# Kernel tuning notes

Hardware: AMD Instinct MI355X
Metric: run time of the kernel (lower is better)

Reference implementation:

```python
import jax, jax.numpy as jnp
import numpy as np

D_MODEL = 512
TEMP = 30.0  # softmax temperature used by TransformerTrack-style RelationUnit
EPS = 1e-5
NORM_SCALE = float(np.sqrt(1.0 / (D_MODEL * 4 * 4)))


def _instance_l2norm(x):
    # x: [n, hw, b, d]; InstanceL2Norm over (dim, h, w) per (image, batch) sample
    n, hw, b, d = x.shape
    ss = jnp.sum(x * x, axis=(1, 3), keepdims=True)  # [n,1,b,1]
    return x * (NORM_SCALE * jnp.sqrt((d * hw) / (ss + EPS)))


def _cnorm(r, i):
    # joint L2 normalization of a complex vector along last axis
    s = jnp.sqrt(jnp.sum(r * r + i * i, axis=-1, keepdims=True) + 1e-12)
    return r / s, i / s


def _rel_self_attn(xr, xi, er, ei, WK):
    # xr/xi: [n, L, b, d]; er/ei: [n, L, L, b, dk] relative (helix) embeddings
    qr, qi = _cnorm(xr @ WK, xi @ WK)           # [n,L,b,dk]
    # real part of complex conjugate inner product <q, k>
    scores = (jnp.einsum('nqbk,nlbk->nbql', qr, qr)
              + jnp.einsum('nqbk,nlbk->nbql', qi, qi)
              + jnp.einsum('nqbk,nqlbk->nbql', qr, er)
              + jnp.einsum('nqbk,nqlbk->nbql', qi, ei))
    A = jax.nn.softmax(scores * TEMP, axis=-1)  # [n,b,q,l]
    out_r = jnp.einsum('nbql,nlbd->nqbd', A, xr)
    out_i = jnp.einsum('nbql,nlbd->nqbd', A, xi)
    return out_r, out_i


def _cross_attn(qr_in, qi_in, kr_in, ki_in, vr, vi, WK):
    # q: [Lq,b,d]; k,v: [Lk,b,d]
    qr, qi = _cnorm(qr_in @ WK, qi_in @ WK)
    kr, ki = _cnorm(kr_in @ WK, ki_in @ WK)
    scores = jnp.einsum('qbk,lbk->bql', qr, kr) + jnp.einsum('qbk,lbk->bql', qi, ki)
    A = jax.nn.softmax(scores * TEMP, axis=-1)
    out_r = jnp.einsum('bql,lbd->qbd', A, vr)
    out_i = jnp.einsum('bql,lbd->qbd', A, vi)
    return out_r, out_i


def _forward(src_real, src_imag, tgt_real, tgt_imag,
             src_emb_real, src_emb_imag, tgt_emb_real, tgt_emb_imag,
             pos_real, pos_imag, WK_rel, WK_cross):
    n, b, d, h, w = src_real.shape
    hw = h * w

    def tok(x):  # [n,b,d,h,w] -> [n,hw,b,d]
        return x.reshape(n, b, d, hw).transpose(0, 3, 1, 2)

    def emb(x):  # [n,b,dk,hw,hw] -> [n,hw,hw,b,dk]
        return x.transpose(0, 3, 4, 1, 2)

    sr, si = tok(src_real), tok(src_imag)
    tr, ti = tok(tgt_real), tok(tgt_imag)
    esr, esi = emb(src_emb_real), emb(src_emb_imag)
    etr, eti = emb(tgt_emb_real), emb(tgt_emb_imag)

    # ---- encoder (num_layers = 1) ----
    s2r, s2i = _rel_self_attn(sr, si, esr, esi, WK_rel)
    mem_r = _instance_l2norm(sr + s2r).reshape(n * hw, b, d)
    mem_i = _instance_l2norm(si + s2i).reshape(n * hw, b, d)

    # pos: [n,b,h,w] -> [n*hw, b, d] (broadcast over dim as in .repeat(1,1,dim))
    pr = jnp.broadcast_to(pos_real.reshape(n, b, hw).transpose(0, 2, 1).reshape(n * hw, b, 1), (n * hw, b, d))
    pi = jnp.broadcast_to(pos_imag.reshape(n, b, hw).transpose(0, 2, 1).reshape(n * hw, b, 1), (n * hw, b, d))

    def IN3(x):
        return _instance_l2norm(x.reshape(n, hw, b, d)).reshape(n * hw, b, d)

    # ---- decoder (num_layers = 1) ----
    t2r, t2i = _rel_self_attn(tr, ti, etr, eti, WK_rel)
    xr = _instance_l2norm(tr + t2r).reshape(n * hw, b, d)
    xi = _instance_l2norm(ti + t2i).reshape(n * hw, b, d)

    mask_r, mask_i = _cross_attn(xr, xi, mem_r, mem_i, pr, pi, WK_cross)
    y2r = IN3(xr * mask_r)
    y2i = IN3(xi * mask_i)

    t3r, t3i = _cross_attn(xr, xi, mem_r, mem_i, mem_r * pr, mem_i * pi, WK_cross)
    y4r = IN3(xr + t3r)
    y4i = IN3(xi + t3i)

    out_r = IN3(y2r + y4r)
    out_i = IN3(y2i + y4i)

    feat_r = out_r.reshape(n, h, w, b, d).transpose(0, 3, 4, 1, 2).reshape(n * b, d, h, w)
    feat_i = out_i.reshape(n, h, w, b, d).transpose(0, 3, 4, 1, 2).reshape(n * b, d, h, w)
    return out_r, out_i, feat_r, feat_i


def setup_inputs() -> dict:
    key = jax.random.key(0)
    ks = jax.random.split(key, 12)
    n, b, d, h, dk = 2, 2, 512, 16, 64
    hw = h * h
    inp = {
        'src_real': jax.random.normal(ks[0], (n, b, d, h, h), jnp.float32),
        'src_imag': jax.random.normal(ks[1], (n, b, d, h, h), jnp.float32),
        'tgt_real': jax.random.normal(ks[2], (n, b, d, h, h), jnp.float32),
        'tgt_imag': jax.random.normal(ks[3], (n, b, d, h, h), jnp.float32),
        'src_emb_real': jax.random.normal(ks[4], (n, b, dk, hw, hw), jnp.float32),
        'src_emb_imag': jax.random.normal(ks[5], (n, b, dk, hw, hw), jnp.float32),
        'tgt_emb_real': jax.random.normal(ks[6], (n, b, dk, hw, hw), jnp.float32),
        'tgt_emb_imag': jax.random.normal(ks[7], (n, b, dk, hw, hw), jnp.float32),
        'pos_real': jax.random.uniform(ks[8], (n, b, h, h), jnp.float32),
        'pos_imag': jax.random.uniform(ks[9], (n, b, h, h), jnp.float32),
        'WK_rel': jax.random.normal(ks[10], (d, dk), jnp.float32) * 0.02,
        'WK_cross': jax.random.normal(ks[11], (d, 128), jnp.float32) * 0.02,
    }
    return inp


def reference(src_real, src_imag, tgt_real, tgt_imag,
              src_emb_real, src_emb_imag, tgt_emb_real, tgt_emb_imag,
              pos_real, pos_imag, WK_rel, WK_cross):
    return _forward(src_real, src_imag, tgt_real, tgt_imag,
                    src_emb_real, src_emb_imag, tgt_emb_real, tgt_emb_imag,
                    pos_real, pos_imag, WK_rel, WK_cross)
```

## Files before the change

### kernel.cpp

```cpp
#include <hip/hip_runtime.h>
#include <cstdint>
#include <cstddef>

#define N_ 2
#define B_ 2
#define D_ 512
#define HW_ 256
#define DK_ 64
#define DKC_ 128
#define G_ 4
#define NBLK_ 32

constexpr size_t OFF_TSR = 0;
constexpr size_t OFF_TSI = 524288;
constexpr size_t OFF_TTR = 1048576;
constexpr size_t OFF_TTI = 1572864;
constexpr size_t OFF_QSR = 2097152;
constexpr size_t OFF_QSI = OFF_QSR + 65536;
constexpr size_t OFF_QTR = OFF_QSI + 65536;
constexpr size_t OFF_QTI = OFF_QTR + 65536;
constexpr size_t OFF_AS  = OFF_QTI + 65536;
constexpr size_t OFF_AT  = OFF_AS + 262144;
constexpr size_t OFF_YSR = OFF_AT + 262144;
constexpr size_t OFF_YSI = OFF_YSR + 524288;
constexpr size_t OFF_YTR = OFF_YSI + 524288;
constexpr size_t OFF_YTI = OFF_YTR + 524288;
constexpr size_t OFF_QCR = OFF_YTI + 524288;
constexpr size_t OFF_QCI = OFF_QCR + 131072;
constexpr size_t OFF_KCR = OFF_QCI + 131072;
constexpr size_t OFF_KCI = OFF_KCR + 131072;
constexpr size_t OFF_AC  = OFF_KCI + 131072;
constexpr size_t OFF_T3R = OFF_AC + 524288;
constexpr size_t OFF_T3I = OFF_T3R + 524288;
constexpr size_t OFF_MR  = OFF_T3I + 524288;
constexpr size_t OFF_MI  = OFF_MR + 1024;
constexpr size_t OFF_P1  = OFF_MI + 1024;
constexpr size_t OFF_P2  = OFF_P1 + 512;
constexpr size_t OFF_P3  = OFF_P2 + 512;
constexpr size_t OFF_S1  = OFF_P3 + 256;
constexpr size_t OFF_S2  = OFF_S1 + 16;
constexpr size_t OFF_SZ  = OFF_S2 + 16;

template<int NT>
__device__ __forceinline__ float blk_sum(float v, float* sh) {
  int tid = threadIdx.x;
  sh[tid] = v; __syncthreads();
  #pragma unroll
  for (int s = NT/2; s > 0; s >>= 1) { if (tid < s) sh[tid] += sh[tid+s]; __syncthreads(); }
  float r = sh[0]; __syncthreads(); return r;
}
template<int NT>
__device__ __forceinline__ float blk_max(float v, float* sh) {
  int tid = threadIdx.x;
  sh[tid] = v; __syncthreads();
  #pragma unroll
  for (int s = NT/2; s > 0; s >>= 1) { if (tid < s) sh[tid] = fmaxf(sh[tid], sh[tid+s]); __syncthreads(); }
  float r = sh[0]; __syncthreads(); return r;
}
__device__ __forceinline__ float wave_max(float v) {
  #pragma unroll
  for (int o = 32; o; o >>= 1) v = fmaxf(v, __shfl_xor(v, o, 64));
  return v;
}
__device__ __forceinline__ float wave_sum(float v) {
  #pragma unroll
  for (int o = 32; o; o >>= 1) v += __shfl_xor(v, o, 64);
  return v;
}

__global__ void k_transpose(const float* sR, const float* sI, const float* tR, const float* tI, float* ws) {
  int which = blockIdx.y;
  const float* in = (which==0)? sR : (which==1)? sI : (which==2)? tR : tI;
  float* out = ws + ((which==0)? OFF_TSR : (which==1)? OFF_TSI : (which==2)? OFF_TTR : OFF_TTI);
  int bx = blockIdx.x;
  int pt = bx & 3, dt = (bx>>2)&7, nb = bx>>5;
  int ni = nb>>1, bi = nb&1;
  __shared__ float tile[64][65];
  int tid = threadIdx.x;
  int p0 = pt*64, d0 = dt*64;
  #pragma unroll
  for (int it=0; it<16; ++it) {
    int i = it*256 + tid; int row = i>>6, col = i&63;
    tile[row][col] = in[(size_t)(nb*D_ + d0+row)*HW_ + p0+col];
  }
  __syncthreads();
  #pragma unroll
  for (int it=0; it<16; ++it) {
    int i = it*256 + tid; int row = i>>6, col = i&63;
    out[(size_t)((ni*HW_ + p0+row)*B_ + bi)*D_ + d0+col] = tile[col][row];
  }
}

__global__ void k_qrel(float* ws, const float* WK) {
  int idx = blockIdx.x;
  int which = idx >> 10; int t = idx & 1023;
  int r = t >> 1, bi = t & 1;
  const float* Tr = ws + (which ? OFF_TTR : OFF_TSR);
  const float* Ti = ws + (which ? OFF_TTI : OFF_TSI);
  float* Qr = ws + (which ? OFF_QTR : OFF_QSR);
  float* Qi = ws + (which ? OFF_QTI : OFF_QSI);
  int tid = threadIdx.x;
  int kk = tid & 63, isIm = tid >> 6;
  const float* x = (isIm ? Ti : Tr) + (size_t)(r*B_ + bi)*D_;
  const float4* x4 = (const float4*)x;
  float acc = 0.f;
  #pragma unroll 8
  for (int d4 = 0; d4 < 128; ++d4) {
    float4 xv = x4[d4]; int d = d4*4;
    acc += xv.x*WK[(d+0)*DK_+kk] + xv.y*WK[(d+1)*DK_+kk] + xv.z*WK[(d+2)*DK_+kk] + xv.w*WK[(d+3)*DK_+kk];
  }
  __shared__ float sh[128];
  float ss = blk_sum<128>(acc*acc, sh);
  float q = acc / sqrtf(ss + 1e-12f);
  (isIm ? Qi : Qr)[(size_t)(r*B_ + bi)*DK_ + kk] = q;
}

__global__ void __launch_bounds__(256) k_selfattn(float* ws, const float* esr, const float* esi,
                                                  const float* etr, const float* eti) {
  int idx = blockIdx.x;
  int qg = idx & 63, nb = (idx>>6)&3, which = idx>>8;
  int ni = nb>>1, bi = nb&1;
  const float* Qr = ws + (which ? OFF_QTR : OFF_QSR);
  const float* Qi = ws + (which ? OFF_QTI : OFF_QSI);
  const float* er = which ? etr : esr;
  const float* ei = which ? eti : esi;
  float* A = ws + (which ? OFF_AT : OFF_AS);
  __shared__ float qq[4][128];
  int tid = threadIdx.x;
  {
    int row = tid>>6, k = tid&63;
    int tok = ni*HW_ + qg*4 + row;
    qq[row][k]    = Qr[(size_t)(tok*B_ + bi)*DK_ + k];
    qq[row][64+k] = Qi[(size_t)(tok*B_ + bi)*DK_ + k];
  }
  __syncthreads();
  int w = tid>>6, lane = tid&63;
  int iq = qg*4 + w;
  int l0 = lane*4;
  float acc[4] = {0.f,0.f,0.f,0.f};
  const float4* qqr4 = (const float4*)&qq[w][0];
  const float4* qqi4 = (const float4*)&qq[w][64];
  #pragma unroll 4
  for (int k4 = 0; k4 < 16; ++k4) {
    float4 qr = qqr4[k4], qi = qqi4[k4];
    #pragma unroll
    for (int j = 0; j < 4; ++j) {
      float4 xr = *(const float4*)&Qr[(size_t)((ni*HW_ + l0+j)*B_ + bi)*DK_ + k4*4];
      float4 xi = *(const float4*)&Qi[(size_t)((ni*HW_ + l0+j)*B_ + bi)*DK_ + k4*4];
      acc[j] += qr.x*xr.x + qr.y*xr.y + qr.z*xr.z + qr.w*xr.w
              + qi.x*xi.x + qi.y*xi.y + qi.z*xi.z + qi.w*xi.w;
    }
  }
  size_t eb = (size_t)nb*4194304 + (size_t)iq*256 + l0;
  #pragma unroll 4
  for (int k = 0; k < 64; ++k) {
    float4 e4r = *(const float4*)&er[eb + (size_t)k*65536];
    float4 e4i = *(const float4*)&ei[eb + (size_t)k*65536];
    float qr = qq[w][k], qi = qq[w][64+k];
    acc[0] += qr*e4r.x + qi*e4i.x;
    acc[1] += qr*e4r.y + qi*e4i.y;
    acc[2] += qr*e4r.z + qi*e4i.z;
    acc[3] += qr*e4r.w + qi*e4i.w;
  }
  float s0 = acc[0]*30.f, s1 = acc[1]*30.f, s2 = acc[2]*30.f, s3 = acc[3]*30.f;
  float m = wave_max(fmaxf(fmaxf(s0,s1), fmaxf(s2,s3)));
  float e0 = __expf(s0-m), e1 = __expf(s1-m), e2 = __expf(s2-m), e3 = __expf(s3-m);
  float inv = 1.f / wave_sum(e0+e1+e2+e3);
  float4 outv = make_float4(e0*inv, e1*inv, e2*inv, e3*inv);
  *(float4*)&A[(size_t)nb*65536 + (size_t)iq*256 + l0] = outv;
}

__global__ void __launch_bounds__(128) k_selfapply(float* ws) {
  int bx = blockIdx.x;
  int dt = bx & 7, qt = (bx>>3)&7, nb = (bx>>6)&3, which = bx>>8;
  int ni = nb>>1, bi = nb&1;
  const float* A  = ws + (which ? OFF_AT : OFF_AS) + (size_t)nb*65536;
  const float* Xr = ws + (which ? OFF_TTR : OFF_TSR);
  const float* Xi = ws + (which ? OFF_TTI : OFF_TSI);
  float* Yr = ws + (which ? OFF_YTR : OFF_YSR);
  float* Yi = ws + (which ? OFF_YTI : OFF_YSI);
  __shared__ float As[32][33], Xrs[32][68], Xis[32][68];
  int tid = threadIdx.x, ty = tid>>4, tx = tid&15;
  int ty4 = ty*4, tx4 = tx*4;
  float ar[4][4] = {}, ai[4][4] = {};
  for (int c = 0; c < 8; ++c) {
    #pragma unroll
    for (int it = 0; it < 8; ++it) {
      int i = it*128 + tid; int row = i>>5, col = i&31;
      As[row][col] = A[(size_t)(qt*32+row)*256 + c*32+col];
    }
    #pragma unroll
    for (int it = 0; it < 16; ++it) {
      int i = it*128 + tid; int row = i>>6, col = i&63;
      size_t xb = (size_t)((ni*HW_ + c*32+row)*B_ + bi)*D_ + dt*64+col;
      Xrs[row][col] = Xr[xb]; Xis[row][col] = Xi[xb];
    }
    __syncthreads();
    #pragma unroll
    for (int kk = 0; kk < 32; ++kk) {
      float4 vr = *(const float4*)&Xrs[kk][tx4];
      float4 vi = *(const float4*)&Xis[kk][tx4];
      #pragma unroll
      for (int i = 0; i < 4; ++i) {
        float a = As[ty4+i][kk];
        ar[i][0] += a*vr.x; ar[i][1] += a*vr.y; ar[i][2] += a*vr.z; ar[i][3] += a*vr.w;
        ai[i][0] += a*vi.x; ai[i][1] += a*vi.y; ai[i][2] += a*vi.z; ai[i][3] += a*vi.w;
      }
    }
    __syncthreads();
  }
  #pragma unroll
  for (int i = 0; i < 4; ++i) {
    size_t o = (size_t)((ni*HW_ + qt*32 + ty4+i)*B_ + bi)*D_ + dt*64 + tx4;
    #pragma unroll
    for (int j = 0; j < 4; ++j) { Yr[o+j] = Xr[o+j] + ar[i][j]; Yi[o+j] = Xi[o+j] + ai[i][j]; }
  }
}

__global__ void k_reduce4(float* ws) {
  int qy = blockIdx.y;
  const float* a = ws + ((qy==0)? OFF_YSR : (qy==1)? OFF_YSI : (qy==2)? OFF_YTR : OFF_YTI);
  int g = blockIdx.x / NBLK_, blk = blockIdx.x % NBLK_;
  int ni = g>>1, bi = g&1;
  int tid = threadIdx.x;
  float acc = 0.f;
  for (int p = blk; p < HW_; p += NBLK_) {
    const float* row = a + (size_t)((ni*HW_ + p)*B_ + bi)*D_;
    for (int d = tid; d < D_; d += 256) { float v = row[d]; acc += v*v; }
  }
  __shared__ float sh[256];
  float s = blk_sum<256>(acc, sh);
  if (!tid) ws[OFF_P1 + (size_t)(qy*G_ + g)*NBLK_ + blk] = s;
}

__global__ void k_finalize(const float* part, float* scales, int nq) {
  int t = threadIdx.x;
  if (t < nq) {
    float ss = 0.f;
    for (int j = 0; j < NBLK_; ++j) ss += part[t*NBLK_ + j];
    scales[t] = 4.f * rsqrtf(ss + 1e-5f);
  }
}

__global__ void k_applyscale(float* ws, const float* scales) {
  int qy = blockIdx.y;
  float* a = ws + ((qy==0)? OFF_YSR : (qy==1)? OFF_YSI : (qy==2)? OFF_YTR : OFF_YTI);
  int idx4 = blockIdx.x*256 + threadIdx.x;
  int elem = idx4*4;
  int bi = (elem / D_) & 1;
  int r = elem >> 10;
  int ni = r >> 8;
  float s = scales[qy*G_ + ni*2 + bi];
  float4 v = ((float4*)a)[idx4];
  v.x *= s; v.y *= s; v.z *= s; v.w *= s;
  ((float4*)a)[idx4] = v;
}

__global__ void k_crossproj(float* ws, const float* W) {
  int idx = blockIdx.x;
  int isK = idx >> 10; int t = idx & 1023;
  int r = t >> 1, bi = t & 1;
  const float* inR = ws + (isK ? OFF_YSR : OFF_YTR);
  const float* inI = ws + (isK ? OFF_YSI : OFF_YTI);
  float* oR = ws + (isK ? OFF_KCR : OFF_QCR);
  float* oI = ws + (isK ? OFF_KCI : OFF_QCI);
  int tid = threadIdx.x;
  const float4* xr4 = (const float4*)(inR + (size_t)(r*B_ + bi)*D_);
  const float4* xi4 = (const float4*)(inI + (size_t)(r*B_ + bi)*D_);
  float aR = 0.f, aI = 0.f;
  #pragma unroll 8
  for (int d4 = 0; d4 < 128; ++d4) {
    float4 rv = xr4[d4], iv = xi4[d4]; int d = d4*4;
    float w0 = W[(d+0)*DKC_ + tid], w1 = W[(d+1)*DKC_ + tid], w2 = W[(d+2)*DKC_ + tid], w3 = W[(d+3)*DKC_ + tid];
    aR += rv.x*w0 + rv.y*w1 + rv.z*w2 + rv.w*w3;
    aI += iv.x*w0 + iv.y*w1 + iv.z*w2 + iv.w*w3;
  }
  __shared__ float sh[128];
  float ss = blk_sum<128>(aR*aR + aI*aI, sh);
  float inv = 1.f / sqrtf(ss + 1e-12f);
  oR[(size_t)(r*B_ + bi)*DKC_ + tid] = aR * inv;
  oI[(size_t)(r*B_ + bi)*DKC_ + tid] = aI * inv;
}

__global__ void __launch_bounds__(128) k_crossscore(float* ws) {
  int bx = blockIdx.x;
  int lt = bx & 7, qt = (bx>>3)&15, bi = bx>>7;
  const float* Qr = ws + OFF_QCR; const float* Qi = ws + OFF_QCI;
  const float* Kr = ws + OFF_KCR; const float* Ki = ws + OFF_KCI;
  float* S = ws + OFF_AC + (size_t)bi*262144;
  __shared__ float Qrs[32][33], Qis[32][33], Krs[32][68], Kis[32][68];
  int tid = threadIdx.x, ty = tid>>4, tx = tid&15;
  int ty4 = ty*4, tx4 = tx*4;
  float acc[4][4] = {};
  for (int c = 0; c < 4; ++c) {
    #pragma unroll
    for (int it = 0; it < 8; ++it) {
      int i = it*128 + tid; int row = i>>5, col = i&31;
      Qrs[row][col] = Qr[(size_t)((qt*32+row)*B_ + bi)*DKC_ + c*32 + col];
      Qis[row][col] = Qi[(size_t)((qt*32+row)*B_ + bi)*DKC_ + c*32 + col];
    }
    #pragma unroll
    for (int it = 0; it < 16; ++it) {
      int i = it*128 + tid; int kk = i&31, col = i>>5;
      Krs[kk][col] = Kr[(size_t)((lt*64+col)*B_ + bi)*DKC_ + c*32 + kk];
      Kis[kk][col] = Ki[(size_t)((lt*64+col)*B_ + bi)*DKC_ + c*32 + kk];
    }
    __syncthreads();
    #pragma unroll
    for (int kk = 0; kk < 32; ++kk) {
      float4 kr = *(const float4*)&Krs[kk][tx4];
      float4 ki = *(const float4*)&Kis[kk][tx4];
      #pragma unroll
      for (int i = 0; i < 4; ++i) {
        float qr = Qrs[ty4+i][kk], qi = Qis[ty4+i][kk];
        acc[i][0] += qr*kr.x + qi*ki.x;
        acc[i][1] += qr*kr.y + qi*ki.y;
        acc[i][2] += qr*kr.z + qi*ki.z;
        acc[i][3] += qr*kr.w + qi*ki.w;
      }
    }
    __syncthreads();
  }
  #pragma unroll
  for (int i = 0; i < 4; ++i)
    #pragma unroll
    for (int j = 0; j < 4; ++j)
      S[(size_t)(qt*32+ty4+i)*512 + lt*64+tx4+j] = acc[i][j];
}

__global__ void k_softmaxrow(float* ws, const float* posr, const float* posi) {
  int bx = blockIdx.x;
  int bi = bx >> 9, iq = bx & 511;
  float* row = ws + OFF_AC + (size_t)bi*262144 + (size_t)iq*512;
  int tid = threadIdx.x;
  float s0 = row[tid]*30.f, s1 = row[tid+256]*30.f;
  __shared__ float sh[256];
  float m = blk_max<256>(fmaxf(s0, s1), sh);
  float e0 = __expf(s0 - m), e1 = __expf(s1 - m);
  float sum = blk_sum<256>(e0 + e1, sh);
  float inv = 1.f / sum;
  float a0 = e0*inv, a1 = e1*inv;
  row[tid] = a0; row[tid+256] = a1;
  float pr0 = posr[bi*HW_ + tid],        pr1 = posr[(B_+bi)*HW_ + tid];
  float pi0 = posi[bi*HW_ + tid],        pi1 = posi[(B_+bi)*HW_ + tid];
  float mr = blk_sum<256>(a0*pr0 + a1*pr1, sh);
  float mi = blk_sum<256>(a0*pi0 + a1*pi1, sh);
  if (!tid) { ws[OFF_MR + bi*512 + iq] = mr; ws[OFF_MI + bi*512 + iq] = mi; }
}

__global__ void __launch_bounds__(128) k_crossapply(float* ws, const float* posr, const float* posi) {
  int bx = blockIdx.x;
  int dt = bx & 7, qt = (bx>>3)&15, bi = (bx>>7)&1, kc = bx>>8;
  const float* A  = ws + OFF_AC + (size_t)bi*262144;
  const float* Mr = ws + OFF_YSR; const float* Mi = ws + OFF_YSI;
  float* Pr = ws + (kc ? OFF_TSR : OFF_T3R);
  float* Pi = ws + (kc ? OFF_TSI : OFF_T3I);
  __shared__ float As[32][33], Vrs[32][68], Vis[32][68];
  int tid = threadIdx.x, ty = tid>>4, tx = tid&15;
  int ty4 = ty*4, tx4 = tx*4;
  float ar[4][4] = {}, ai[4][4] = {};
  for (int c = 0; c < 8; ++c) {
    int kb = kc*256 + c*32;
    #pragma unroll
    for (int it = 0; it < 8; ++it) {
      int i = it*128 + tid; int row = i>>5, col = i&31;
      As[row][col] = A[(size_t)(qt*32+row)*512 + kb+col];
    }
    #pragma unroll
    for (int it = 0; it < 16; ++it) {
      int i = it*128 + tid; int row = i>>6, col = i&63;
      int l = kb + row; int nil = l>>8, pl = l&255;
      float pvr = posr[(nil*B_ + bi)*HW_ + pl];
      float pvi = posi[(nil*B_ + bi)*HW_ + pl];
      size_t vb = (size_t)(l*B_ + bi)*D_ + dt*64+col;
      Vrs[row][col] = Mr[vb] * pvr;
      Vis[row][col] = Mi[vb] * pvi;
    }
    __syncthreads();
    #pragma unroll
    for (int kk = 0; kk < 32; ++kk) {
      float4 vr = *(const float4*)&Vrs[kk][tx4];
      float4 vi = *(const float4*)&Vis[kk][tx4];
      #pragma unroll
      for (int i = 0; i < 4; ++i) {
        float a = As[ty4+i][kk];
        ar[i][0] += a*vr.x; ar[i][1] += a*vr.y; ar[i][2] += a*vr.z; ar[i][3] += a*vr.w;
        ai[i][0] += a*vi.x; ai[i][1] += a*vi.y; ai[i][2] += a*vi.z; ai[i][3] += a*vi.w;
      }
    }
    __syncthreads();
  }
  #pragma unroll
  for (int i = 0; i < 4; ++i) {
    size_t o = (size_t)((qt*32+ty4+i)*B_ + bi)*D_ + dt*64 + tx4;
    #pragma unroll
    for (int j = 0; j < 4; ++j) { Pr[o+j] = ar[i][j]; Pi[o+j] = ai[i][j]; }
  }
}

__global__ void k_reducey24(float* ws) {
  int qy = blockIdx.y;
  int g = blockIdx.x / NBLK_, blk = blockIdx.x % NBLK_;
  int ni = g>>1, bi = g&1;
  const float* X   = ws + ((qy==0 || qy==2) ? OFF_YTR : OFF_YTI);
  const float* T3a = ws + ((qy==2) ? OFF_T3R : OFF_T3I);
  const float* T3b = ws + ((qy==2) ? OFF_TSR : OFF_TSI);
  const float* M   = ws + ((qy==0) ? OFF_MR : OFF_MI);
  int tid = threadIdx.x;
  float acc = 0.f;
  for (int p = blk; p < HW_; p += NBLK_) {
    int l = ni*HW_ + p;
    size_t rb = (size_t)(l*B_ + bi)*D_;
    if (qy < 2) {
      float m = M[bi*512 + l];
      for (int d = tid; d < D_; d += 256) { float v = X[rb+d]*m; acc += v*v; }
    } else {
      for (int d = tid; d < D_; d += 256) { float v = X[rb+d] + T3a[rb+d] + T3b[rb+d]; acc += v*v; }
    }
  }
  __shared__ float sh[256];
  float s = blk_sum<256>(acc, sh);
  if (!tid) ws[OFF_P2 + (size_t)(qy*G_ + g)*NBLK_ + blk] = s;
}

__global__ void k_combine(float* ws, const float* scales2) {
  int y = blockIdx.y;
  int g = blockIdx.x / NBLK_, blk = blockIdx.x % NBLK_;
  int ni = g>>1, bi = g&1;
  const float* X   = ws + (y ? OFF_YTI : OFF_YTR);
  float* T3a       = ws + (y ? OFF_T3I : OFF_T3R);
  const float* T3b = ws + (y ? OFF_TSI : OFF_TSR);
  const float* M   = ws + (y ? OFF_MI : OFF_MR);
  float a2 = scales2[y*G_ + g], a4 = scales2[(2+y)*G_ + g];
  int tid = threadIdx.x;
  float acc = 0.f;
  for (int p = blk; p < HW_; p += NBLK_) {
    int l = ni*HW_ + p;
    float m = M[bi*512 + l];
    size_t rb = (size_t)(l*B_ + bi)*D_;
    for (int d = tid; d < D_; d += 256) {
      float x = X[rb+d];
      float z = a2*(x*m) + a4*(x + T3a[rb+d] + T3b[rb+d]);
      T3a[rb+d] = z;
      acc += z*z;
    }
  }
  __shared__ float sh[256];
  float s = blk_sum<256>(acc, sh);
  if (!tid) ws[OFF_P3 + (size_t)(y*G_ + g)*NBLK_ + blk] = s;
}

__global__ void k_final(float* ws, const float* scalesZ, float* out) {
  int y = blockIdx.y;
  int bx = blockIdx.x;
  int pt = bx & 3, dt = (bx>>2)&7, nb = bx>>5;
  int ni = nb>>1, bi = nb&1;
  const float* Z = ws + (y ? OFF_T3I : OFF_T3R);
  float s = scalesZ[y*G_ + nb];
  float* o1 = out + (size_t)y*524288;
  float* o2 = out + (size_t)(2+y)*524288;
  __shared__ float tile[64][65];
  int tid = threadIdx.x;
  int p0 = pt*64, d0 = dt*64;
  #pragma unroll
  for (int it = 0; it < 16; ++it) {
    int i = it*256 + tid; int row = i>>6, col = i&63;
    size_t idx = (size_t)((ni*HW_ + p0+row)*B_ + bi)*D_ + d0+col;
    float v = Z[idx] * s;
    o1[idx] = v;
    tile[row][col] = v;
  }
  __syncthreads();
  #pragma unroll
  for (int it = 0; it < 16; ++it) {
    int i = it*256 + tid; int row = i>>6, col = i&63;
    o2[(size_t)(nb*D_ + d0+row)*HW_ + p0+col] = tile[col][row];
  }
}

extern "C" void kernel_launch(void* const* d_in, const int* in_sizes, int n_in,
                              void* d_out, int out_size, void* d_ws, size_t ws_size,
                              hipStream_t stream) {
  const float* srcR = (const float*)d_in[0];
  const float* srcI = (const float*)d_in[1];
  const float* tgtR = (const float*)d_in[2];
  const float* tgtI = (const float*)d_in[3];
  const float* esr  = (const float*)d_in[4];
  const float* esi  = (const float*)d_in[5];
  const float* etr  = (const float*)d_in[6];
  const float* eti  = (const float*)d_in[7];
  const float* posR = (const float*)d_in[8];
  const float* posI = (const float*)d_in[9];
  const float* WKrel   = (const float*)d_in[10];
  const float* WKcross = (const float*)d_in[11];
  float* ws  = (float*)d_ws;
  float* out = (float*)d_out;

  k_transpose <<<dim3(128,4), 256, 0, stream>>>(srcR, srcI, tgtR, tgtI, ws);
  k_qrel      <<<2048, 128, 0, stream>>>(ws, WKrel);
  k_selfattn  <<<512, 256, 0, stream>>>(ws, esr, esi, etr, eti);
  k_selfapply <<<512, 128, 0, stream>>>(ws);
  k_reduce4   <<<dim3(G_*NBLK_,4), 256, 0, stream>>>(ws);
  k_finalize  <<<1, 64, 0, stream>>>(ws + OFF_P1, ws + OFF_S1, 16);
  k_applyscale<<<dim3(512,4), 256, 0, stream>>>(ws, ws + OFF_S1);
  k_crossproj <<<2048, 128, 0, stream>>>(ws, WKcross);
  k_crossscore<<<256, 128, 0, stream>>>(ws);
  k_softmaxrow<<<1024, 256, 0, stream>>>(ws, posR, posI);
  k_crossapply<<<512, 128, 0, stream>>>(ws, posR, posI);
  k_reducey24 <<<dim3(G_*NBLK_,4), 256, 0, stream>>>(ws);
  k_finalize  <<<1, 64, 0, stream>>>(ws + OFF_P2, ws + OFF_S2, 16);
  k_combine   <<<dim3(G_*NBLK_,2), 256, 0, stream>>>(ws, ws + OFF_S2);
  k_finalize  <<<1, 64, 0, stream>>>(ws + OFF_P3, ws + OFF_SZ, 8);
  k_final     <<<dim3(128,2), 256, 0, stream>>>(ws, ws + OFF_SZ, out);
}
```

Measured before the change: 281.3 us.

## Split self-attention score into tiled Gram kernel and split-K embedding kernel

```diff
diff --git a/kernel.cpp b/kernel.cpp
--- a/kernel.cpp
+++ b/kernel.cpp
@@ -57,16 +57,6 @@
   for (int s = NT/2; s > 0; s >>= 1) { if (tid < s) sh[tid] = fmaxf(sh[tid], sh[tid+s]); __syncthreads(); }
   float r = sh[0]; __syncthreads(); return r;
 }
-__device__ __forceinline__ float wave_max(float v) {
-  #pragma unroll
-  for (int o = 32; o; o >>= 1) v = fmaxf(v, __shfl_xor(v, o, 64));
-  return v;
-}
-__device__ __forceinline__ float wave_sum(float v) {
-  #pragma unroll
-  for (int o = 32; o; o >>= 1) v += __shfl_xor(v, o, 64);
-  return v;
-}
 
 __global__ void k_transpose(const float* sR, const float* sI, const float* tR, const float* tI, float* ws) {
   int which = blockIdx.y;
@@ -115,59 +105,92 @@
   (isIm ? Qi : Qr)[(size_t)(r*B_ + bi)*DK_ + kk] = q;
 }
 
+__global__ void __launch_bounds__(128) k_gram(float* ws) {
+  int bx = blockIdx.x;
+  int lt = bx & 3, qt = (bx>>2)&7, nb = (bx>>5)&3, which = bx>>7;
+  int ni = nb>>1, bi = nb&1;
+  const float* Qr = ws + (which ? OFF_QTR : OFF_QSR);
+  const float* Qi = ws + (which ? OFF_QTI : OFF_QSI);
+  float* A = ws + (which ? OFF_AT : OFF_AS) + (size_t)nb*65536;
+  __shared__ float Qrs[32][33], Qis[32][33], Krs[32][68], Kis[32][68];
+  int tid = threadIdx.x, ty = tid>>4, tx = tid&15;
+  int ty4 = ty*4, tx4 = tx*4;
+  float acc[4][4] = {};
+  for (int c = 0; c < 2; ++c) {
+    #pragma unroll
+    for (int it = 0; it < 8; ++it) {
+      int i = it*128 + tid; int row = i>>5, col = i&31;
+      size_t qa = (size_t)((ni*HW_ + qt*32+row)*B_ + bi)*DK_ + c*32 + col;
+      Qrs[row][col] = Qr[qa];
+      Qis[row][col] = Qi[qa];
+    }
+    #pragma unroll
+    for (int it = 0; it < 16; ++it) {
+      int i = it*128 + tid; int kk = i&31, col = i>>5;
+      size_t ka = (size_t)((ni*HW_ + lt*64+col)*B_ + bi)*DK_ + c*32 + kk;
+      Krs[kk][col] = Qr[ka];
+      Kis[kk][col] = Qi[ka];
+    }
+    __syncthreads();
+    #pragma unroll
+    for (int kk = 0; kk < 32; ++kk) {
+      float4 kr = *(const float4*)&Krs[kk][tx4];
+      float4 ki = *(const float4*)&Kis[kk][tx4];
+      #pragma unroll
+      for (int i = 0; i < 4; ++i) {
+        float qr = Qrs[ty4+i][kk], qi = Qis[ty4+i][kk];
+        acc[i][0] += qr*kr.x + qi*ki.x;
+        acc[i][1] += qr*kr.y + qi*ki.y;
+        acc[i][2] += qr*kr.z + qi*ki.z;
+        acc[i][3] += qr*kr.w + qi*ki.w;
+      }
+    }
+    __syncthreads();
+  }
+  #pragma unroll
+  for (int i = 0; i < 4; ++i)
+    #pragma unroll
+    for (int j = 0; j < 4; ++j)
+      A[(size_t)(qt*32+ty4+i)*256 + lt*64+tx4+j] = acc[i][j];
+}
+
 __global__ void __launch_bounds__(256) k_selfattn(float* ws, const float* esr, const float* esi,
                                                   const float* etr, const float* eti) {
   int idx = blockIdx.x;
-  int qg = idx & 63, nb = (idx>>6)&3, which = idx>>8;
+  int iq = idx & 255, nb = (idx>>8)&3, which = idx>>10;
   int ni = nb>>1, bi = nb&1;
   const float* Qr = ws + (which ? OFF_QTR : OFF_QSR);
   const float* Qi = ws + (which ? OFF_QTI : OFF_QSI);
   const float* er = which ? etr : esr;
   const float* ei = which ? eti : esi;
-  float* A = ws + (which ? OFF_AT : OFF_AS);
-  __shared__ float qq[4][128];
-  int tid = threadIdx.x;
-  {
-    int row = tid>>6, k = tid&63;
-    int tok = ni*HW_ + qg*4 + row;
-    qq[row][k]    = Qr[(size_t)(tok*B_ + bi)*DK_ + k];
-    qq[row][64+k] = Qi[(size_t)(tok*B_ + bi)*DK_ + k];
-  }
+  float* Arow = ws + (which ? OFF_AT : OFF_AS) + (size_t)nb*65536 + (size_t)iq*256;
+  int tid = threadIdx.x, w = tid>>6, lane = tid&63;
+  size_t qbase = (size_t)((ni*HW_ + iq)*B_ + bi)*DK_ + w*16;
+  int kl = lane & 15;
+  float qv = ((lane & 16) ? Qi : Qr)[qbase + kl];
+  int l0 = lane*4;
+  float a0=0.f, a1=0.f, a2=0.f, a3=0.f;
+  size_t eb = (size_t)nb*4194304 + (size_t)(w*16)*65536 + (size_t)iq*256 + l0;
+  #pragma unroll 4
+  for (int kk = 0; kk < 16; ++kk) {
+    float4 e4r = *(const float4*)&er[eb + (size_t)kk*65536];
+    float4 e4i = *(const float4*)&ei[eb + (size_t)kk*65536];
+    float fr = __shfl(qv, kk);
+    float fi = __shfl(qv, 16+kk);
+    a0 += fr*e4r.x + fi*e4i.x;
+    a1 += fr*e4r.y + fi*e4i.y;
+    a2 += fr*e4r.z + fi*e4i.z;
+    a3 += fr*e4r.w + fi*e4i.w;
+  }
+  __shared__ float part[4][256];
+  __shared__ float sh[256];
+  *(float4*)&part[w][l0] = make_float4(a0,a1,a2,a3);
   __syncthreads();
-  int w = tid>>6, lane = tid&63;
-  int iq = qg*4 + w;
-  int l0 = lane*4;
-  float acc[4] = {0.f,0.f,0.f,0.f};
-  const float4* qqr4 = (const float4*)&qq[w][0];
-  const float4* qqi4 = (const float4*)&qq[w][64];
-  #pragma unroll 4
-  for (int k4 = 0; k4 < 16; ++k4) {
-    float4 qr = qqr4[k4], qi = qqi4[k4];
-    #pragma unroll
-    for (int j = 0; j < 4; ++j) {
-      float4 xr = *(const float4*)&Qr[(size_t)((ni*HW_ + l0+j)*B_ + bi)*DK_ + k4*4];
-      float4 xi = *(const float4*)&Qi[(size_t)((ni*HW_ + l0+j)*B_ + bi)*DK_ + k4*4];
-      acc[j] += qr.x*xr.x + qr.y*xr.y + qr.z*xr.z + qr.w*xr.w
-              + qi.x*xi.x + qi.y*xi.y + qi.z*xi.z + qi.w*xi.w;
-    }
-  }
-  size_t eb = (size_t)nb*4194304 + (size_t)iq*256 + l0;
-  #pragma unroll 4
-  for (int k = 0; k < 64; ++k) {
-    float4 e4r = *(const float4*)&er[eb + (size_t)k*65536];
-    float4 e4i = *(const float4*)&ei[eb + (size_t)k*65536];
-    float qr = qq[w][k], qi = qq[w][64+k];
-    acc[0] += qr*e4r.x + qi*e4i.x;
-    acc[1] += qr*e4r.y + qi*e4i.y;
-    acc[2] += qr*e4r.z + qi*e4i.z;
-    acc[3] += qr*e4r.w + qi*e4i.w;
-  }
-  float s0 = acc[0]*30.f, s1 = acc[1]*30.f, s2 = acc[2]*30.f, s3 = acc[3]*30.f;
-  float m = wave_max(fmaxf(fmaxf(s0,s1), fmaxf(s2,s3)));
-  float e0 = __expf(s0-m), e1 = __expf(s1-m), e2 = __expf(s2-m), e3 = __expf(s3-m);
-  float inv = 1.f / wave_sum(e0+e1+e2+e3);
-  float4 outv = make_float4(e0*inv, e1*inv, e2*inv, e3*inv);
-  *(float4*)&A[(size_t)nb*65536 + (size_t)iq*256 + l0] = outv;
+  float s = (part[0][tid]+part[1][tid]+part[2][tid]+part[3][tid] + Arow[tid]) * 30.f;
+  float m = blk_max<256>(s, sh);
+  float e = __expf(s - m);
+  float sum = blk_sum<256>(e, sh);
+  Arow[tid] = e / sum;
 }
 
 __global__ void __launch_bounds__(128) k_selfapply(float* ws) {
@@ -498,7 +521,8 @@
 
   k_transpose <<<dim3(128,4), 256, 0, stream>>>(srcR, srcI, tgtR, tgtI, ws);
   k_qrel      <<<2048, 128, 0, stream>>>(ws, WKrel);
-  k_selfattn  <<<512, 256, 0, stream>>>(ws, esr, esi, etr, eti);
+  k_gram      <<<256, 128, 0, stream>>>(ws);
+  k_selfattn  <<<2048, 256, 0, stream>>>(ws, esr, esi, etr, eti);
   k_selfapply <<<512, 128, 0, stream>>>(ws);
   k_reduce4   <<<dim3(G_*NBLK_,4), 256, 0, stream>>>(ws);
   k_finalize  <<<1, 64, 0, stream>>>(ws + OFF_P1, ws + OFF_S1, 16);
```

Measured after the change: 275.0 us. 2.3% less time.
